# Performance work log

Measured on AMD Instinct MI355X. Metric: run time of the kernel, lower is better.

Reference implementation:

```python
import jax, jax.numpy as jnp
import numpy as np

# Module constants from init_kwargs: z_max=32, ppm=2 -> delta=0.5, z_min=0.5, scale_range=[0,9]
Z_MAX = 32.0
DELTA = 0.5  # 1/ppm
Z_MIN = 0.5
SCALE_MIN, SCALE_MAX = 0.0, 9.0
DEPTH_STEPS = np.arange(Z_MIN, Z_MAX + DELTA, DELTA, dtype=np.float32)  # [D=64]


def setup_inputs() -> dict:
    key = jax.random.key(0)
    k1, k2, k3 = jax.random.split(key, 3)
    B, C, H, W, S = 16, 128, 64, 256, 32
    image = jax.random.normal(k1, (B, C, H, W), jnp.float32)
    pixel_scales = jax.random.normal(k2, (B, H, W, S), jnp.float32)
    # focal lengths (fx, fy) in pixels, in [200, 600)
    camera_f = jax.random.uniform(k3, (B, 2), jnp.float32, minval=200.0, maxval=600.0)
    return {"image": image, "pixel_scales": pixel_scales, "camera_f": camera_f}


def _sample_depth_scores(pixel_scales, camera_f):
    # pixel_scales: [B, H, W, S]; camera_f: [B, 2]
    # scale_steps = f_y / depth_steps.flip(-1)
    steps = jnp.asarray(DEPTH_STEPS)[::-1]                      # [D]
    scale_steps = camera_f[:, 1:2] / steps[None, :]             # [B, D]
    g = (jnp.log2(scale_steps) - SCALE_MIN) / (SCALE_MAX - SCALE_MIN) * 2.0 - 1.0  # grid y in [-1,1]
    S = pixel_scales.shape[-1]
    # grid_sample(align_corners=True, padding=zeros), 1D linear interp along scale axis S
    pos = (g + 1.0) * 0.5 * (S - 1)                             # [B, D] in pixel coords
    i0f = jnp.floor(pos)
    w1 = (pos - i0f)[:, None, None, :]                          # [B,1,1,D]
    i0 = i0f.astype(jnp.int32)
    i1 = i0 + 1
    idx0 = jnp.clip(i0, 0, S - 1)[:, None, None, :]             # [B,1,1,D]
    idx1 = jnp.clip(i1, 0, S - 1)[:, None, None, :]
    v0 = jnp.take_along_axis(pixel_scales, jnp.broadcast_to(idx0, pixel_scales.shape[:3] + (i0.shape[-1],)), axis=-1)
    v1 = jnp.take_along_axis(pixel_scales, jnp.broadcast_to(idx1, pixel_scales.shape[:3] + (i1.shape[-1],)), axis=-1)
    m0 = ((i0 >= 0) & (i0 <= S - 1)).astype(pixel_scales.dtype)[:, None, None, :]  # zero padding
    m1 = ((i1 >= 0) & (i1 <= S - 1)).astype(pixel_scales.dtype)[:, None, None, :]
    return v0 * (1.0 - w1) * m0 + v1 * w1 * m1                  # [B, H, W, D]


def reference(image, pixel_scales, camera_f):
    # image: [B, C, H, W]
    depth_scores = _sample_depth_scores(pixel_scales, camera_f)   # [B, H, W, D]
    depth_prob = jax.nn.softmax(depth_scores, axis=1)             # softmax over image rows H
    image_polar = jnp.einsum('bchw,bhwd->bcdw', image, depth_prob)  # [B, C, D, W]
    return image_polar
```

## Files before the change

### kernel.cpp

```cpp
#include <hip/hip_runtime.h>


#define B 16
#define C 128
#define H 64
#define W 256
#define S 32
#define D 64

typedef _Float16 half8 __attribute__((ext_vector_type(8)));

__global__ __launch_bounds__(256) void ppd_scores_kernel(
    const float* __restrict__ ps,
    const float* __restrict__ camf,
    _Float16* __restrict__ E)
{
    const int d = threadIdx.x & 63;
    const int w = (blockIdx.x << 2) + (threadIdx.x >> 6);
    const int b = blockIdx.y;

    const float fy   = camf[b * 2 + 1];
    const float step = 32.0f - 0.5f * (float)d;
    const float g    = log2f(fy / step) / 9.0f * 2.0f - 1.0f;
    const float pos  = (g + 1.0f) * 0.5f * (float)(S - 1);
    const float fi0  = floorf(pos);
    const float w1   = pos - fi0;
    const int   i0   = (int)fi0;
    const int   i1   = i0 + 1;
    const float m0   = (i0 >= 0 && i0 <= S - 1) ? 1.0f : 0.0f;
    const float m1   = (i1 >= 0 && i1 <= S - 1) ? 1.0f : 0.0f;
    const float c0   = (1.0f - w1) * m0;
    const float c1   = w1 * m1;
    const int idx0   = min(max(i0, 0), S - 1);
    const int idx1   = min(max(i1, 0), S - 1);

    const float* __restrict__ row = ps + ((size_t)b * H * W + w) * S;

    float sc[H];
#pragma unroll
    for (int h = 0; h < H; ++h) {
        const float* r = row + (size_t)h * (W * S);
        sc[h] = r[idx0] * c0 + r[idx1] * c1;
    }

    float mx = sc[0];
#pragma unroll
    for (int h = 1; h < H; ++h) mx = fmaxf(mx, sc[h]);

    float sum = 0.0f;
#pragma unroll
    for (int h = 0; h < H; ++h) {
        sc[h] = expf(sc[h] - mx);
        sum += sc[h];
    }
    const float invZ = 1.0f / sum;

    _Float16* __restrict__ eout = E + ((size_t)b * H * W + w) * D + d;
#pragma unroll
    for (int h = 0; h < H; ++h)
        __builtin_nontemporal_store((_Float16)(sc[h] * invZ),
                                    eout + (size_t)h * (W * D));
}

__global__ __launch_bounds__(256) void ppd_gemm_kernel(
    const float* __restrict__ img,
    const _Float16* __restrict__ E,
    float* __restrict__ out)
{
    const int bid = blockIdx.x;
    const int swz = (bid & 7) * (2048 / 8) + (bid >> 3);
    const int dt = swz & 3;
    const int ct = (swz >> 2) & 7;
    const int wt = (swz >> 5) & 3;
    const int b  = swz >> 7;

    const int w  = (wt << 6) + (threadIdx.x & 63);
    const int g  = threadIdx.x >> 6;
    const int c0 = (ct << 4) + (g << 2);
    const int d0 = dt << 4;

    const float* __restrict__ ip = img + ((size_t)b * C + c0) * (H * W) + w;
    const _Float16* __restrict__ ep = E + ((size_t)b * H * W + w) * D + d0;

    float acc[4][16];
#pragma unroll
    for (int i = 0; i < 4; ++i)
#pragma unroll
        for (int j = 0; j < 16; ++j) acc[i][j] = 0.0f;

#pragma unroll 2
    for (int h = 0; h < H; ++h) {
        float iv[4];
#pragma unroll
        for (int i = 0; i < 4; ++i)
            iv[i] = ip[((size_t)i * H + h) * W];

        const half8* evp = (const half8*)(ep + (size_t)h * (W * D));
        const half8 ev0 = evp[0];
        const half8 ev1 = evp[1];
        float pv[16];
#pragma unroll
        for (int j = 0; j < 8; ++j) {
            pv[j]     = (float)ev0[j];
            pv[j + 8] = (float)ev1[j];
        }

#pragma unroll
        for (int i = 0; i < 4; ++i)
#pragma unroll
            for (int j = 0; j < 16; ++j)
                acc[i][j] = fmaf(iv[i], pv[j], acc[i][j]);
    }

#pragma unroll
    for (int i = 0; i < 4; ++i) {
        float* __restrict__ op = out + (((size_t)b * C + c0 + i) * D + d0) * W + w;
#pragma unroll
        for (int j = 0; j < 16; ++j)
            __builtin_nontemporal_store(acc[i][j], op + (size_t)j * W);
    }
}

extern "C" void kernel_launch(void* const* d_in, const int* in_sizes, int n_in,
                              void* d_out, int out_size, void* d_ws, size_t ws_size,
                              hipStream_t stream) {
    const float* img  = (const float*)d_in[0];
    const float* ps   = (const float*)d_in[1];
    const float* camf = (const float*)d_in[2];
    float* out = (float*)d_out;

    _Float16* E = (_Float16*)d_ws;

    ppd_scores_kernel<<<dim3(W / 4, B), 256, 0, stream>>>(ps, camf, E);
    ppd_gemm_kernel<<<2048, 256, 0, stream>>>(img, E, out);
}
```

Baseline: 435.5 us.

## Split softmax into stats and weights kernels with coalesced h-paired E layout

Replaces the single scores kernel with two passes: one computes the per-(b,d,w) max and inverse sum while recomputing scores rather than holding 64 in registers, and one stages pixel_scales tiles in LDS and writes normalized weights. E is re-laid out as [B,H/2,D,W] with two h values packed per half2 element, so stores and the GEMM's loads are contiguous along w. The GEMM now consumes two h rows per iteration from this layout. This costs an extra kernel launch, a second read of pixel_scales, and extra Mv/Iz traffic, in exchange for lower register pressure and better memory coalescing.

```diff
diff --git a/kernel.cpp b/kernel.cpp
--- a/kernel.cpp
+++ b/kernel.cpp
@@ -7,19 +7,14 @@
 #define W 256
 #define S 32
 #define D 64
-
-typedef _Float16 half8 __attribute__((ext_vector_type(8)));
-
-__global__ __launch_bounds__(256) void ppd_scores_kernel(
-    const float* __restrict__ ps,
-    const float* __restrict__ camf,
-    _Float16* __restrict__ E)
-{
-    const int d = threadIdx.x & 63;
-    const int w = (blockIdx.x << 2) + (threadIdx.x >> 6);
-    const int b = blockIdx.y;
-
-    const float fy   = camf[b * 2 + 1];
+#define HP 32
+
+typedef _Float16 half2v __attribute__((ext_vector_type(2)));
+typedef float float4v __attribute__((ext_vector_type(4)));
+
+__device__ __forceinline__ void interp_coefs(float fy, int d,
+    int& idx0, int& idx1, float& c0, float& c1)
+{
     const float step = 32.0f - 0.5f * (float)d;
     const float g    = log2f(fy / step) / 9.0f * 2.0f - 1.0f;
     const float pos  = (g + 1.0f) * 0.5f * (float)(S - 1);
@@ -29,46 +24,108 @@
     const int   i1   = i0 + 1;
     const float m0   = (i0 >= 0 && i0 <= S - 1) ? 1.0f : 0.0f;
     const float m1   = (i1 >= 0 && i1 <= S - 1) ? 1.0f : 0.0f;
-    const float c0   = (1.0f - w1) * m0;
-    const float c1   = w1 * m1;
-    const int idx0   = min(max(i0, 0), S - 1);
-    const int idx1   = min(max(i1, 0), S - 1);
+    c0 = (1.0f - w1) * m0;
+    c1 = w1 * m1;
+    idx0 = min(max(i0, 0), S - 1);
+    idx1 = min(max(i1, 0), S - 1);
+}
+
+__global__ __launch_bounds__(256) void ppd_mz_kernel(
+    const float* __restrict__ ps,
+    const float* __restrict__ camf,
+    float* __restrict__ Mv,
+    float* __restrict__ Iz)
+{
+    const int d = threadIdx.x & 63;
+    const int w = (blockIdx.x << 2) + (threadIdx.x >> 6);
+    const int b = blockIdx.y;
+
+    int idx0, idx1; float c0, c1;
+    interp_coefs(camf[b * 2 + 1], d, idx0, idx1, c0, c1);
 
     const float* __restrict__ row = ps + ((size_t)b * H * W + w) * S;
 
-    float sc[H];
-#pragma unroll
+    float mx = -1e30f;
+#pragma unroll 8
     for (int h = 0; h < H; ++h) {
         const float* r = row + (size_t)h * (W * S);
-        sc[h] = r[idx0] * c0 + r[idx1] * c1;
-    }
-
-    float mx = sc[0];
-#pragma unroll
-    for (int h = 1; h < H; ++h) mx = fmaxf(mx, sc[h]);
-
+        mx = fmaxf(mx, r[idx0] * c0 + r[idx1] * c1);
+    }
     float sum = 0.0f;
-#pragma unroll
+#pragma unroll 8
     for (int h = 0; h < H; ++h) {
-        sc[h] = expf(sc[h] - mx);
-        sum += sc[h];
-    }
-    const float invZ = 1.0f / sum;
-
-    _Float16* __restrict__ eout = E + ((size_t)b * H * W + w) * D + d;
-#pragma unroll
-    for (int h = 0; h < H; ++h)
-        __builtin_nontemporal_store((_Float16)(sc[h] * invZ),
-                                    eout + (size_t)h * (W * D));
+        const float* r = row + (size_t)h * (W * S);
+        sum += expf(r[idx0] * c0 + r[idx1] * c1 - mx);
+    }
+    const size_t o = ((size_t)b * D + d) * W + w;
+    Mv[o] = mx;
+    Iz[o] = 1.0f / sum;
+}
+
+__global__ __launch_bounds__(256) void ppd_weights_kernel(
+    const float* __restrict__ ps,
+    const float* __restrict__ camf,
+    const float* __restrict__ Mv,
+    const float* __restrict__ Iz,
+    half2v* __restrict__ E)
+{
+    __shared__ float lds[2 * 64 * 33];
+
+    const int t  = threadIdx.x;
+    const int wt = blockIdx.x;
+    const int hp = blockIdx.y;
+    const int b  = blockIdx.z;
+    const int w0 = wt << 6;
+    const int h0 = hp << 1;
+
+    {
+        const int wi = t >> 2, sec = t & 3;
+        const float* gsrc = ps + (((size_t)b * H + h0) * W + w0 + wi) * S + sec * 8;
+        float4v a0 = *(const float4v*)(gsrc);
+        float4v a1 = *(const float4v*)(gsrc + 4);
+        float4v b0 = *(const float4v*)(gsrc + (size_t)W * S);
+        float4v b1 = *(const float4v*)(gsrc + (size_t)W * S + 4);
+        float* d0p = &lds[wi * 33 + sec * 8];
+        float* d1p = d0p + 64 * 33;
+#pragma unroll
+        for (int k = 0; k < 4; ++k) {
+            d0p[k] = a0[k]; d0p[k + 4] = a1[k];
+            d1p[k] = b0[k]; d1p[k + 4] = b1[k];
+        }
+    }
+    __syncthreads();
+
+    const int wl = t & 63;
+    const int w  = w0 + wl;
+    const int wg = t >> 6;
+    const float fy = camf[b * 2 + 1];
+    const float* r0 = &lds[wl * 33];
+    const float* r1 = r0 + 64 * 33;
+
+#pragma unroll
+    for (int dd = 0; dd < 16; ++dd) {
+        const int d = (wg << 4) + dd;
+        int idx0, idx1; float c0, c1;
+        interp_coefs(fy, d, idx0, idx1, c0, c1);
+        const size_t mzo = ((size_t)b * D + d) * W + w;
+        const float m  = Mv[mzo];
+        const float iz = Iz[mzo];
+        const float s0 = r0[idx0] * c0 + r0[idx1] * c1;
+        const float s1 = r1[idx0] * c0 + r1[idx1] * c1;
+        half2v pk;
+        pk[0] = (_Float16)(expf(s0 - m) * iz);
+        pk[1] = (_Float16)(expf(s1 - m) * iz);
+        E[(((size_t)b * HP + hp) * D + d) * W + w] = pk;
+    }
 }
 
 __global__ __launch_bounds__(256) void ppd_gemm_kernel(
     const float* __restrict__ img,
-    const _Float16* __restrict__ E,
+    const half2v* __restrict__ E,
     float* __restrict__ out)
 {
     const int bid = blockIdx.x;
-    const int swz = (bid & 7) * (2048 / 8) + (bid >> 3);
+    const int swz = (bid & 7) * 256 + (bid >> 3);
     const int dt = swz & 3;
     const int ct = (swz >> 2) & 7;
     const int wt = (swz >> 5) & 3;
@@ -79,8 +136,9 @@
     const int c0 = (ct << 4) + (g << 2);
     const int d0 = dt << 4;
 
-    const float* __restrict__ ip = img + ((size_t)b * C + c0) * (H * W) + w;
-    const _Float16* __restrict__ ep = E + ((size_t)b * H * W + w) * D + d0;
+    const float*  __restrict__ ip = img + ((size_t)b * C + c0) * (H * W) + w;
+    const half2v* __restrict__ ep = E + ((size_t)b * HP) * (D * W)
+                                      + (size_t)d0 * W + w;
 
     float acc[4][16];
 #pragma unroll
@@ -89,27 +147,30 @@
         for (int j = 0; j < 16; ++j) acc[i][j] = 0.0f;
 
 #pragma unroll 2
-    for (int h = 0; h < H; ++h) {
-        float iv[4];
+    for (int hp = 0; hp < HP; ++hp) {
+        float iv0[4], iv1[4];
+#pragma unroll
+        for (int i = 0; i < 4; ++i) {
+            iv0[i] = ip[((size_t)i * H + 2 * hp) * W];
+            iv1[i] = ip[((size_t)i * H + 2 * hp + 1) * W];
+        }
+        float pv0[16], pv1[16];
+#pragma unroll
+        for (int j = 0; j < 16; ++j) {
+            half2v e = ep[(size_t)hp * (D * W) + j * W];
+            pv0[j] = (float)e[0];
+            pv1[j] = (float)e[1];
+        }
 #pragma unroll
         for (int i = 0; i < 4; ++i)
-            iv[i] = ip[((size_t)i * H + h) * W];
-
-        const half8* evp = (const half8*)(ep + (size_t)h * (W * D));
-        const half8 ev0 = evp[0];
-        const half8 ev1 = evp[1];
-        float pv[16];
-#pragma unroll
-        for (int j = 0; j < 8; ++j) {
-            pv[j]     = (float)ev0[j];
-            pv[j + 8] = (float)ev1[j];
-        }
-
+#pragma unroll
+            for (int j = 0; j < 16; ++j)
+                acc[i][j] = fmaf(iv0[i], pv0[j], acc[i][j]);
 #pragma unroll
         for (int i = 0; i < 4; ++i)
 #pragma unroll
             for (int j = 0; j < 16; ++j)
-                acc[i][j] = fmaf(iv[i], pv[j], acc[i][j]);
+                acc[i][j] = fmaf(iv1[i], pv1[j], acc[i][j]);
     }
 
 #pragma unroll
@@ -129,8 +190,11 @@
     const float* camf = (const float*)d_in[2];
     float* out = (float*)d_out;
 
-    _Float16* E = (_Float16*)d_ws;
-
-    ppd_scores_kernel<<<dim3(W / 4, B), 256, 0, stream>>>(ps, camf, E);
+    half2v* E  = (half2v*)d_ws;
+    float*  Mv = (float*)((char*)d_ws + (size_t)B * HP * D * W * sizeof(half2v));
+    float*  Iz = Mv + (size_t)B * D * W;
+
+    ppd_mz_kernel<<<dim3(W / 4, B), 256, 0, stream>>>(ps, camf, Mv, Iz);
+    ppd_weights_kernel<<<dim3(W / 64, HP, B), 256, 0, stream>>>(ps, camf, Mv, Iz, E);
     ppd_gemm_kernel<<<2048, 256, 0, stream>>>(img, E, out);
 }
```

Result: faster. 375.8 us (-13.7%).
